# Kernel tuning notes

Hardware: AMD Instinct MI355X
Metric: run time of the kernel (lower is better)

The kernel has to match this reference:

```python
import jax, jax.numpy as jnp
import numpy as np

N, A, B, K = 100000, 64, 128, 27  # active sites, in/out channels, 3^3 offsets
EPS = 1e-4  # scn BatchNorm default eps
LEAK = 0.0  # leakiness=0 -> ReLU


def bn_lrelu(x, gamma, beta):
    # training-mode BN over active sites, fused leaky relu
    mu = x.mean(0)
    var = x.var(0)
    xh = (x - mu) * jax.lax.rsqrt(var + EPS) * gamma + beta
    return jnp.where(xh > 0, xh, LEAK * xh)


def subconv(f, nbr, mask, W):
    # submanifold conv via rulebook: f [N,Cin], nbr [N,K], mask [N,K], W [K,Cin,Cout]
    out = jnp.zeros((f.shape[0], W.shape[2]), f.dtype)
    for k in range(W.shape[0]):  # fixed small set of kernel offsets
        g = jnp.where(mask[:, k:k + 1], f[nbr[:, k]], jnp.zeros((), f.dtype))
        out = out + g @ W[k]
    return out


def setup_inputs() -> dict:
    key = jax.random.key(0)
    ks = jax.random.split(key, 8)
    feat = jax.random.normal(ks[0], (N, A), jnp.float32)
    nbr = jax.random.randint(ks[1], (N, K), 0, N, jnp.int32)
    mask = jax.random.randint(ks[2], (N, K), 0, 2, jnp.int32).astype(bool)
    # self-connection at center offset is always valid in submanifold conv
    center = K // 2
    nbr = nbr.at[:, center].set(jnp.arange(N, dtype=jnp.int32))
    mask = mask.at[:, center].set(True)
    s1 = 1.0 / np.sqrt(K * A)
    s2 = 1.0 / np.sqrt(K * B)
    W1 = jax.random.normal(ks[3], (K, A, B), jnp.float32) * s1
    W2 = jax.random.normal(ks[4], (K, B, B), jnp.float32) * s2
    Wnin = jax.random.normal(ks[5], (A, B), jnp.float32) / np.sqrt(A)
    gamma1 = jnp.ones((A,), jnp.float32)
    beta1 = jnp.zeros((A,), jnp.float32)
    gamma2 = jnp.ones((B,), jnp.float32)
    beta2 = jnp.zeros((B,), jnp.float32)
    return {"feat": feat, "gamma1": gamma1, "beta1": beta1, "W1": W1,
            "gamma2": gamma2, "beta2": beta2, "W2": W2, "Wnin": Wnin,
            "nbr": nbr, "mask": mask}


def reference(feat, gamma1, beta1, W1, gamma2, beta2, W2, Wnin, nbr, mask):
    y1 = feat @ Wnin  # NetworkInNetwork shortcut (a != b)
    h = bn_lrelu(feat, gamma1, beta1)
    h = subconv(h, nbr, mask, W1)
    h = bn_lrelu(h, gamma2, beta2)
    y2 = subconv(h, nbr, mask, W2)
    return y1 + y2  # add_feature_planes
```

## Files before the change

### kernel.cpp

```cpp
#include <hip/hip_runtime.h>
#include <stdint.h>

#define CA 64
#define CB 128
#define KOFF 27
#define BN_EPS 1e-4f

typedef short bf16x8 __attribute__((ext_vector_type(8)));
typedef float f32x4 __attribute__((ext_vector_type(4)));
typedef unsigned int u32x4 __attribute__((ext_vector_type(4)));
typedef unsigned short u16x4 __attribute__((ext_vector_type(4)));

__device__ __forceinline__ unsigned short f2bf(float f) {
  union { float f; uint32_t u; } c; c.f = f;
  uint32_t u = c.u;
  return (unsigned short)((u + 0x7FFFu + ((u >> 16) & 1u)) >> 16);
}

__device__ __forceinline__ void barrier_lds() {
  asm volatile("s_waitcnt lgkmcnt(0)\n\ts_barrier" ::: "memory");
}

__global__ void detect_mask_k(const unsigned char* __restrict__ m, int* flag) {
  unsigned v = 0;
  for (int i = threadIdx.x; i < 4096; i += 256)
    if (i & 3) v |= m[i];
  if (v) atomicOr(flag, 1);
}

__global__ void pack_mask_k(const void* __restrict__ mp, const int* __restrict__ flag,
                            uint32_t* __restrict__ bits, int n) {
  int i = blockIdx.x * blockDim.x + threadIdx.x;
  if (i >= n) return;
  uint32_t b = 0;
  if (*flag) {
    const unsigned char* m = (const unsigned char*)mp + (size_t)i * KOFF;
    for (int k = 0; k < KOFF; k++) b |= (m[k] ? 1u : 0u) << k;
  } else {
    const int* m = (const int*)mp + (size_t)i * KOFF;
    for (int k = 0; k < KOFF; k++) b |= (m[k] ? 1u : 0u) << k;
  }
  bits[i] = b;
}

__global__ void transpose_all_k(const float* __restrict__ W1, const float* __restrict__ W2,
                                const float* __restrict__ Wnin,
                                unsigned short* __restrict__ w1t, unsigned short* __restrict__ w2t,
                                unsigned short* __restrict__ wnt) {
  const int t1 = KOFF * CA * CB, t2 = KOFF * CB * CB, t3 = CA * CB;
  int idx = blockIdx.x * blockDim.x + threadIdx.x;
  if (idx < t1) {
    int ci = idx % CA; int r = idx / CA; int co = r % CB; int k = r / CB;
    w1t[idx] = f2bf(W1[((size_t)k * CA + ci) * CB + co]);
  } else if (idx < t1 + t2) {
    int j = idx - t1;
    int ci = j % CB; int r = j / CB; int co = r % CB; int k = r / CB;
    w2t[j] = f2bf(W2[((size_t)k * CB + ci) * CB + co]);
  } else if (idx < t1 + t2 + t3) {
    int j = idx - t1 - t2;
    int ci = j % CA; int co = j / CA;
    wnt[j] = f2bf(Wnin[(size_t)ci * CB + co]);
  }
}

template<int C>
__global__ void col_stats_k(const float* __restrict__ x, int n, float* __restrict__ sums) {
  __shared__ float ssum[C], ssq[C];
  int t = threadIdx.x;
  for (int i = t; i < C; i += 256) { ssum[i] = 0.f; ssq[i] = 0.f; }
  __syncthreads();
  const int c = t % C;
  const int rpb = 256 / C;
  float s = 0.f, q = 0.f;
  for (int r = blockIdx.x * rpb + t / C; r < n; r += gridDim.x * rpb) {
    float v = x[(size_t)r * C + c];
    s += v; q += v * v;
  }
  atomicAdd(&ssum[c], s);
  atomicAdd(&ssq[c], q);
  __syncthreads();
  for (int i = t; i < C; i += 256) {
    atomicAdd(&sums[i], ssum[i]);
    atomicAdd(&sums[C + i], ssq[i]);
  }
}

template<int C>
__global__ void bn_finalize_k(const float* __restrict__ sums, const float* __restrict__ gamma,
                              const float* __restrict__ beta, float* __restrict__ sc, int n) {
  int c = threadIdx.x;
  if (c >= C) return;
  float inv_n = 1.f / (float)n;
  float mean = sums[c] * inv_n;
  float var = sums[C + c] * inv_n - mean * mean;
  float rstd = rsqrtf(var + BN_EPS);
  float scale = gamma[c] * rstd;
  sc[c] = scale;
  sc[C + c] = beta[c] - mean * scale;
}

template<int C, bool RAW>
__global__ void bn_apply_k(const float* __restrict__ x, const float* __restrict__ sc,
                           unsigned short* __restrict__ h, unsigned short* __restrict__ raw,
                           int total) {
  int idx = (blockIdx.x * blockDim.x + threadIdx.x) * 4;
  if (idx >= total) return;
  f32x4 v = *(const f32x4*)&x[idx];
  int c0 = idx % C;
  u16x4 ho, ro;
#pragma unroll
  for (int j = 0; j < 4; j++) {
    float s = sc[c0 + j], b = sc[C + c0 + j];
    float hv = fmaxf(v[j] * s + b, 0.f);
    ho[j] = f2bf(hv);
    if (RAW) ro[j] = f2bf(v[j]);
  }
  *(u16x4*)&h[idx] = ho;
  if (RAW) *(u16x4*)&raw[idx] = ro;
}

template<int CIN, bool FUSE>
__launch_bounds__(256)
__global__ void conv_k(const unsigned short* __restrict__ hin,
                       const unsigned short* __restrict__ wt,
                       const int* __restrict__ nbr,
                       const uint32_t* __restrict__ mbits,
                       const unsigned short* __restrict__ fbraw,
                       const unsigned short* __restrict__ wnt,
                       float* __restrict__ out, int n) {
  constexpr int TR = 64;
  constexpr int STR = CIN + 8;
  constexpr int FSTR = CA + 8;
  constexpr int NKS = CIN / 32;
  constexpr int CH = CIN / 8;
  constexpr int NP = TR * CH / 256;

  __shared__ alignas(16) unsigned short tile[2][TR * STR];
  __shared__ alignas(16) unsigned short ftile[FUSE ? TR * FSTR : 16];
  __shared__ int lnbr[TR * KOFF];
  __shared__ uint32_t lmb[TR];

  const int t = threadIdx.x;
  const int rowbase = blockIdx.x * TR;
  const int nrows = min(TR, n - rowbase);

  for (int i = t; i < nrows * KOFF; i += 256) lnbr[i] = nbr[(size_t)rowbase * KOFF + i];
  if (t < TR) lmb[t] = (t < nrows) ? mbits[rowbase + t] : 0u;

  if constexpr (FUSE) {
#pragma unroll
    for (int p = 0; p < 2; p++) {
      int r = p * 32 + (t >> 3);
      int ch = (t & 7) * 8;
      u32x4 v = {0, 0, 0, 0};
      if (r < nrows) v = *(const u32x4*)&fbraw[(size_t)(rowbase + r) * CA + ch];
      *(u32x4*)&ftile[r * FSTR + ch] = v;
    }
  }
  __syncthreads();

  const int lane = t & 63;
  const int wave = t >> 6;
  const int l16 = lane & 15;
  const int quad = lane >> 4;
  const int colbase = wave * 32;
  const int goff = (t % CH) * 8;
  const int grow = t / CH;
  const int boff0 = (colbase + l16) * CIN + quad * 8;
  const int boff1 = boff0 + 16 * CIN;

  f32x4 acc[4][2];
#pragma unroll
  for (int i = 0; i < 4; i++) { acc[i][0] = f32x4{0,0,0,0}; acc[i][1] = f32x4{0,0,0,0}; }

  bf16x8 bfr[2][2 * NKS];
  u32x4 gr[NP];

#pragma unroll
  for (int ks = 0; ks < NKS; ks++) {
    bfr[0][2 * ks]     = *(const bf16x8*)&wt[boff0 + ks * 32];
    bfr[0][2 * ks + 1] = *(const bf16x8*)&wt[boff1 + ks * 32];
  }
#pragma unroll
  for (int p = 0; p < NP; p++) {
    int r = p * (256 / CH) + grow;
    u32x4 v = {0, 0, 0, 0};
    if (r < nrows && (lmb[r] & 1u)) v = *(const u32x4*)&hin[(size_t)lnbr[r * KOFF] * CIN + goff];
    gr[p] = v;
  }
#pragma unroll
  for (int p = 0; p < NP; p++) {
    int r = p * (256 / CH) + grow;
    *(u32x4*)&tile[0][r * STR + goff] = gr[p];
  }
  {
    const unsigned short* wk = wt + (size_t)1 * CB * CIN;
#pragma unroll
    for (int ks = 0; ks < NKS; ks++) {
      bfr[1][2 * ks]     = *(const bf16x8*)&wk[boff0 + ks * 32];
      bfr[1][2 * ks + 1] = *(const bf16x8*)&wk[boff1 + ks * 32];
    }
  }
#pragma unroll
  for (int p = 0; p < NP; p++) {
    int r = p * (256 / CH) + grow;
    u32x4 v = {0, 0, 0, 0};
    if (r < nrows && ((lmb[r] >> 1) & 1u))
      v = *(const u32x4*)&hin[(size_t)lnbr[r * KOFF + 1] * CIN + goff];
    gr[p] = v;
  }

  if constexpr (FUSE) {
#pragma unroll
    for (int ks = 0; ks < CA / 32; ks++) {
      bf16x8 b0 = *(const bf16x8*)&wnt[(colbase + l16) * CA + ks * 32 + quad * 8];
      bf16x8 b1 = *(const bf16x8*)&wnt[(colbase + 16 + l16) * CA + ks * 32 + quad * 8];
#pragma unroll
      for (int rt = 0; rt < 4; rt++) {
        bf16x8 a = *(const bf16x8*)&ftile[(rt * 16 + l16) * FSTR + ks * 32 + quad * 8];
        acc[rt][0] = __builtin_amdgcn_mfma_f32_16x16x32_bf16(a, b0, acc[rt][0], 0, 0, 0);
        acc[rt][1] = __builtin_amdgcn_mfma_f32_16x16x32_bf16(a, b1, acc[rt][1], 0, 0, 0);
      }
    }
  }
  barrier_lds();

#pragma unroll
  for (int k = 0; k < KOFF; k++) {
    const int cur = k & 1, nxt = cur ^ 1;
#pragma unroll
    for (int ks = 0; ks < NKS; ks++) {
#pragma unroll
      for (int rt = 0; rt < 4; rt++) {
        bf16x8 a = *(const bf16x8*)&tile[cur][(rt * 16 + l16) * STR + ks * 32 + quad * 8];
        acc[rt][0] = __builtin_amdgcn_mfma_f32_16x16x32_bf16(a, bfr[cur][2 * ks],     acc[rt][0], 0, 0, 0);
        acc[rt][1] = __builtin_amdgcn_mfma_f32_16x16x32_bf16(a, bfr[cur][2 * ks + 1], acc[rt][1], 0, 0, 0);
      }
    }
    if (k + 2 < KOFF) {
      const unsigned short* wk = wt + (size_t)(k + 2) * CB * CIN;
#pragma unroll
      for (int ks = 0; ks < NKS; ks++) {
        bfr[cur][2 * ks]     = *(const bf16x8*)&wk[boff0 + ks * 32];
        bfr[cur][2 * ks + 1] = *(const bf16x8*)&wk[boff1 + ks * 32];
      }
    }
    if (k + 1 < KOFF) {
#pragma unroll
      for (int p = 0; p < NP; p++) {
        int r = p * (256 / CH) + grow;
        *(u32x4*)&tile[nxt][r * STR + goff] = gr[p];
      }
      if (k + 2 < KOFF) {
#pragma unroll
        for (int p = 0; p < NP; p++) {
          int r = p * (256 / CH) + grow;
          u32x4 v = {0, 0, 0, 0};
          if (r < nrows && ((lmb[r] >> (k + 2)) & 1u))
            v = *(const u32x4*)&hin[(size_t)lnbr[r * KOFF + k + 2] * CIN + goff];
          gr[p] = v;
        }
      }
      barrier_lds();
    }
  }

#pragma unroll
  for (int rt = 0; rt < 4; rt++) {
#pragma unroll
    for (int ct = 0; ct < 2; ct++) {
#pragma unroll
      for (int i = 0; i < 4; i++) {
        int r = rt * 16 + quad * 4 + i;
        if (r < nrows) {
          int c = colbase + ct * 16 + l16;
          out[(size_t)(rowbase + r) * CB + c] = acc[rt][ct][i];
        }
      }
    }
  }
}

extern "C" void kernel_launch(void* const* d_in, const int* in_sizes, int n_in,
                              void* d_out, int out_size, void* d_ws, size_t ws_size,
                              hipStream_t stream) {
  const float* feat   = (const float*)d_in[0];
  const float* gamma1 = (const float*)d_in[1];
  const float* beta1  = (const float*)d_in[2];
  const float* W1     = (const float*)d_in[3];
  const float* gamma2 = (const float*)d_in[4];
  const float* beta2  = (const float*)d_in[5];
  const float* W2     = (const float*)d_in[6];
  const float* Wnin   = (const float*)d_in[7];
  const int*   nbr    = (const int*)d_in[8];
  const void*  mask   = d_in[9];
  float* out = (float*)d_out;

  const int n = in_sizes[0] / CA;

  char* ws = (char*)d_ws;
  size_t off = 0;
  auto alloc = [&](size_t bytes) { size_t p = off; off += (bytes + 255) & ~(size_t)255; return p; };
  int*            flag  = (int*)           (ws + alloc(256));
  float*          sums1 = (float*)         (ws + alloc(2 * CA * 4));
  float*          sums2 = (float*)         (ws + alloc(2 * CB * 4));
  float*          sc1   = (float*)         (ws + alloc(2 * CA * 4));
  float*          sc2   = (float*)         (ws + alloc(2 * CB * 4));
  uint32_t*       mbits = (uint32_t*)      (ws + alloc((size_t)n * 4));
  unsigned short* fb    = (unsigned short*)(ws + alloc((size_t)n * CA * 2));
  unsigned short* hb1   = (unsigned short*)(ws + alloc((size_t)n * CA * 2));
  float*          out1  = (float*)         (ws + alloc((size_t)n * CB * 4));
  unsigned short* hb2   = (unsigned short*)(ws + alloc((size_t)n * CB * 2));
  unsigned short* w1t   = (unsigned short*)(ws + alloc((size_t)KOFF * CB * CA * 2));
  unsigned short* w2t   = (unsigned short*)(ws + alloc((size_t)KOFF * CB * CB * 2));
  unsigned short* wnt   = (unsigned short*)(ws + alloc((size_t)CB * CA * 2));

  hipMemsetAsync(d_ws, 0, 1792, stream);

  detect_mask_k<<<1, 256, 0, stream>>>((const unsigned char*)mask, flag);
  pack_mask_k<<<(n + 255) / 256, 256, 0, stream>>>(mask, flag, mbits, n);

  {
    int tot = KOFF * CA * CB + KOFF * CB * CB + CA * CB;
    transpose_all_k<<<(tot + 255) / 256, 256, 0, stream>>>(W1, W2, Wnin, w1t, w2t, wnt);
  }

  col_stats_k<CA><<<256, 256, 0, stream>>>(feat, n, sums1);
  bn_finalize_k<CA><<<1, CA, 0, stream>>>(sums1, gamma1, beta1, sc1, n);
  bn_apply_k<CA, true><<<(n * CA / 4 + 255) / 256, 256, 0, stream>>>(feat, sc1, hb1, fb, n * CA);

  conv_k<CA, false><<<(n + 63) / 64, 256, 0, stream>>>(hb1, w1t, nbr, mbits, nullptr, nullptr, out1, n);

  col_stats_k<CB><<<256, 256, 0, stream>>>(out1, n, sums2);
  bn_finalize_k<CB><<<1, CB, 0, stream>>>(sums2, gamma2, beta2, sc2, n);
  bn_apply_k<CB, false><<<(n * CB / 4 + 255) / 256, 256, 0, stream>>>(out1, sc2, hb2, nullptr, n * CB);

  conv_k<CB, true><<<(n + 63) / 64, 256, 0, stream>>>(hb2, w2t, nbr, mbits, fb, wnt, out, n);
}
```

Measured before the change: 531.1 us.

## Replace mask bits with zero-row sentinel indices and deepen gather prefetch to four offsets

```diff
diff --git a/kernel.cpp b/kernel.cpp
--- a/kernel.cpp
+++ b/kernel.cpp
@@ -28,19 +28,20 @@
   if (v) atomicOr(flag, 1);
 }
 
-__global__ void pack_mask_k(const void* __restrict__ mp, const int* __restrict__ flag,
-                            uint32_t* __restrict__ bits, int n) {
+__global__ void make_nbr_eff_k(const int* __restrict__ nbr, const void* __restrict__ mp,
+                               const int* __restrict__ flag, int* __restrict__ ne, int n) {
   int i = blockIdx.x * blockDim.x + threadIdx.x;
-  if (i >= n) return;
-  uint32_t b = 0;
-  if (*flag) {
-    const unsigned char* m = (const unsigned char*)mp + (size_t)i * KOFF;
-    for (int k = 0; k < KOFF; k++) b |= (m[k] ? 1u : 0u) << k;
-  } else {
-    const int* m = (const int*)mp + (size_t)i * KOFF;
-    for (int k = 0; k < KOFF; k++) b |= (m[k] ? 1u : 0u) << k;
-  }
-  bits[i] = b;
+  if (i >= n * KOFF) return;
+  bool m = (*flag) ? (((const unsigned char*)mp)[i] != 0)
+                   : (((const int*)mp)[i] != 0);
+  ne[i] = m ? nbr[i] : n;
+}
+
+__global__ void zero_rows_k(unsigned short* hb1, unsigned short* fb,
+                            unsigned short* hb2, int n) {
+  int i = threadIdx.x;
+  if (i < CA) { hb1[(size_t)n * CA + i] = 0; fb[(size_t)n * CA + i] = 0; }
+  if (i < CB) { hb2[(size_t)n * CB + i] = 0; }
 }
 
 __global__ void transpose_all_k(const float* __restrict__ W1, const float* __restrict__ W2,
@@ -123,39 +124,26 @@
 __launch_bounds__(256)
 __global__ void conv_k(const unsigned short* __restrict__ hin,
                        const unsigned short* __restrict__ wt,
-                       const int* __restrict__ nbr,
-                       const uint32_t* __restrict__ mbits,
+                       const int* __restrict__ nbr_eff,
                        const unsigned short* __restrict__ fbraw,
                        const unsigned short* __restrict__ wnt,
                        float* __restrict__ out, int n) {
   constexpr int TR = 64;
   constexpr int STR = CIN + 8;
-  constexpr int FSTR = CA + 8;
   constexpr int NKS = CIN / 32;
   constexpr int CH = CIN / 8;
   constexpr int NP = TR * CH / 256;
 
   __shared__ alignas(16) unsigned short tile[2][TR * STR];
-  __shared__ alignas(16) unsigned short ftile[FUSE ? TR * FSTR : 16];
   __shared__ int lnbr[TR * KOFF];
-  __shared__ uint32_t lmb[TR];
 
   const int t = threadIdx.x;
   const int rowbase = blockIdx.x * TR;
   const int nrows = min(TR, n - rowbase);
 
-  for (int i = t; i < nrows * KOFF; i += 256) lnbr[i] = nbr[(size_t)rowbase * KOFF + i];
-  if (t < TR) lmb[t] = (t < nrows) ? mbits[rowbase + t] : 0u;
-
-  if constexpr (FUSE) {
-#pragma unroll
-    for (int p = 0; p < 2; p++) {
-      int r = p * 32 + (t >> 3);
-      int ch = (t & 7) * 8;
-      u32x4 v = {0, 0, 0, 0};
-      if (r < nrows) v = *(const u32x4*)&fbraw[(size_t)(rowbase + r) * CA + ch];
-      *(u32x4*)&ftile[r * FSTR + ch] = v;
-    }
+  for (int i = t; i < TR * KOFF; i += 256) {
+    int r = i / KOFF;
+    lnbr[i] = (rowbase + r < n) ? nbr_eff[(size_t)rowbase * KOFF + i] : n;
   }
   __syncthreads();
 
@@ -174,40 +162,24 @@
   for (int i = 0; i < 4; i++) { acc[i][0] = f32x4{0,0,0,0}; acc[i][1] = f32x4{0,0,0,0}; }
 
   bf16x8 bfr[2][2 * NKS];
-  u32x4 gr[NP];
-
+  u32x4 gr[4][NP];
+
+#pragma unroll
+  for (int j = 0; j < 4; j++) {
+#pragma unroll
+    for (int p = 0; p < NP; p++) {
+      int r = p * (256 / CH) + grow;
+      int idx = lnbr[r * KOFF + j];
+      gr[j][p] = *(const u32x4*)&hin[(size_t)idx * CIN + goff];
+    }
+  }
 #pragma unroll
   for (int ks = 0; ks < NKS; ks++) {
     bfr[0][2 * ks]     = *(const bf16x8*)&wt[boff0 + ks * 32];
     bfr[0][2 * ks + 1] = *(const bf16x8*)&wt[boff1 + ks * 32];
-  }
-#pragma unroll
-  for (int p = 0; p < NP; p++) {
-    int r = p * (256 / CH) + grow;
-    u32x4 v = {0, 0, 0, 0};
-    if (r < nrows && (lmb[r] & 1u)) v = *(const u32x4*)&hin[(size_t)lnbr[r * KOFF] * CIN + goff];
-    gr[p] = v;
-  }
-#pragma unroll
-  for (int p = 0; p < NP; p++) {
-    int r = p * (256 / CH) + grow;
-    *(u32x4*)&tile[0][r * STR + goff] = gr[p];
-  }
-  {
-    const unsigned short* wk = wt + (size_t)1 * CB * CIN;
-#pragma unroll
-    for (int ks = 0; ks < NKS; ks++) {
-      bfr[1][2 * ks]     = *(const bf16x8*)&wk[boff0 + ks * 32];
-      bfr[1][2 * ks + 1] = *(const bf16x8*)&wk[boff1 + ks * 32];
-    }
-  }
-#pragma unroll
-  for (int p = 0; p < NP; p++) {
-    int r = p * (256 / CH) + grow;
-    u32x4 v = {0, 0, 0, 0};
-    if (r < nrows && ((lmb[r] >> 1) & 1u))
-      v = *(const u32x4*)&hin[(size_t)lnbr[r * KOFF + 1] * CIN + goff];
-    gr[p] = v;
+    const unsigned short* wk = wt + (size_t)CB * CIN;
+    bfr[1][2 * ks]     = *(const bf16x8*)&wk[boff0 + ks * 32];
+    bfr[1][2 * ks + 1] = *(const bf16x8*)&wk[boff1 + ks * 32];
   }
 
   if constexpr (FUSE) {
@@ -217,17 +189,24 @@
       bf16x8 b1 = *(const bf16x8*)&wnt[(colbase + 16 + l16) * CA + ks * 32 + quad * 8];
 #pragma unroll
       for (int rt = 0; rt < 4; rt++) {
-        bf16x8 a = *(const bf16x8*)&ftile[(rt * 16 + l16) * FSTR + ks * 32 + quad * 8];
+        int g = rowbase + rt * 16 + l16; g = (g < n) ? g : n;
+        bf16x8 a = *(const bf16x8*)&fbraw[(size_t)g * CA + ks * 32 + quad * 8];
         acc[rt][0] = __builtin_amdgcn_mfma_f32_16x16x32_bf16(a, b0, acc[rt][0], 0, 0, 0);
         acc[rt][1] = __builtin_amdgcn_mfma_f32_16x16x32_bf16(a, b1, acc[rt][1], 0, 0, 0);
       }
     }
   }
+
+#pragma unroll
+  for (int p = 0; p < NP; p++) {
+    int r = p * (256 / CH) + grow;
+    *(u32x4*)&tile[0][r * STR + goff] = gr[0][p];
+  }
   barrier_lds();
 
 #pragma unroll
   for (int k = 0; k < KOFF; k++) {
-    const int cur = k & 1, nxt = cur ^ 1;
+    const int cur = k & 1;
 #pragma unroll
     for (int ks = 0; ks < NKS; ks++) {
 #pragma unroll
@@ -237,6 +216,14 @@
         acc[rt][1] = __builtin_amdgcn_mfma_f32_16x16x32_bf16(a, bfr[cur][2 * ks + 1], acc[rt][1], 0, 0, 0);
       }
     }
+    if (k + 4 < KOFF) {
+#pragma unroll
+      for (int p = 0; p < NP; p++) {
+        int r = p * (256 / CH) + grow;
+        int idx = lnbr[r * KOFF + (k + 4)];
+        gr[(k + 4) & 3][p] = *(const u32x4*)&hin[(size_t)idx * CIN + goff];
+      }
+    }
     if (k + 2 < KOFF) {
       const unsigned short* wk = wt + (size_t)(k + 2) * CB * CIN;
 #pragma unroll
@@ -249,17 +236,7 @@
 #pragma unroll
       for (int p = 0; p < NP; p++) {
         int r = p * (256 / CH) + grow;
-        *(u32x4*)&tile[nxt][r * STR + goff] = gr[p];
-      }
-      if (k + 2 < KOFF) {
-#pragma unroll
-        for (int p = 0; p < NP; p++) {
-          int r = p * (256 / CH) + grow;
-          u32x4 v = {0, 0, 0, 0};
-          if (r < nrows && ((lmb[r] >> (k + 2)) & 1u))
-            v = *(const u32x4*)&hin[(size_t)lnbr[r * KOFF + k + 2] * CIN + goff];
-          gr[p] = v;
-        }
+        *(u32x4*)&tile[(k + 1) & 1][r * STR + goff] = gr[(k + 1) & 3][p];
       }
       barrier_lds();
     }
@@ -306,11 +283,11 @@
   float*          sums2 = (float*)         (ws + alloc(2 * CB * 4));
   float*          sc1   = (float*)         (ws + alloc(2 * CA * 4));
   float*          sc2   = (float*)         (ws + alloc(2 * CB * 4));
-  uint32_t*       mbits = (uint32_t*)      (ws + alloc((size_t)n * 4));
-  unsigned short* fb    = (unsigned short*)(ws + alloc((size_t)n * CA * 2));
-  unsigned short* hb1   = (unsigned short*)(ws + alloc((size_t)n * CA * 2));
+  int*            neff  = (int*)           (ws + alloc((size_t)n * KOFF * 4));
+  unsigned short* fb    = (unsigned short*)(ws + alloc((size_t)(n + 1) * CA * 2));
+  unsigned short* hb1   = (unsigned short*)(ws + alloc((size_t)(n + 1) * CA * 2));
   float*          out1  = (float*)         (ws + alloc((size_t)n * CB * 4));
-  unsigned short* hb2   = (unsigned short*)(ws + alloc((size_t)n * CB * 2));
+  unsigned short* hb2   = (unsigned short*)(ws + alloc((size_t)(n + 1) * CB * 2));
   unsigned short* w1t   = (unsigned short*)(ws + alloc((size_t)KOFF * CB * CA * 2));
   unsigned short* w2t   = (unsigned short*)(ws + alloc((size_t)KOFF * CB * CB * 2));
   unsigned short* wnt   = (unsigned short*)(ws + alloc((size_t)CB * CA * 2));
@@ -318,7 +295,8 @@
   hipMemsetAsync(d_ws, 0, 1792, stream);
 
   detect_mask_k<<<1, 256, 0, stream>>>((const unsigned char*)mask, flag);
-  pack_mask_k<<<(n + 255) / 256, 256, 0, stream>>>(mask, flag, mbits, n);
+  make_nbr_eff_k<<<(n * KOFF + 255) / 256, 256, 0, stream>>>(nbr, mask, flag, neff, n);
+  zero_rows_k<<<1, 256, 0, stream>>>(hb1, fb, hb2, n);
 
   {
     int tot = KOFF * CA * CB + KOFF * CB * CB + CA * CB;
@@ -329,11 +307,11 @@
   bn_finalize_k<CA><<<1, CA, 0, stream>>>(sums1, gamma1, beta1, sc1, n);
   bn_apply_k<CA, true><<<(n * CA / 4 + 255) / 256, 256, 0, stream>>>(feat, sc1, hb1, fb, n * CA);
 
-  conv_k<CA, false><<<(n + 63) / 64, 256, 0, stream>>>(hb1, w1t, nbr, mbits, nullptr, nullptr, out1, n);
+  conv_k<CA, false><<<(n + 63) / 64, 256, 0, stream>>>(hb1, w1t, neff, nullptr, nullptr, out1, n);
 
   col_stats_k<CB><<<256, 256, 0, stream>>>(out1, n, sums2);
   bn_finalize_k<CB><<<1, CB, 0, stream>>>(sums2, gamma2, beta2, sc2, n);
   bn_apply_k<CB, false><<<(n * CB / 4 + 255) / 256, 256, 0, stream>>>(out1, sc2, hb2, nullptr, n * CB);
 
-  conv_k<CB, true><<<(n + 63) / 64, 256, 0, stream>>>(hb2, w2t, nbr, mbits, fb, wnt, out, n);
-}
+  conv_k<CB, true><<<(n + 63) / 64, 256, 0, stream>>>(hb2, w2t, neff, fb, wnt, out, n);
+}
```

Result: slower. 544.7 us (+2.6%).
